# Performance work log

Hardware: AMD Instinct MI355X
Metric: run time of the kernel (lower is better)

The kernel has to match this reference:

```python
import jax, jax.numpy as jnp
import numpy as np


def _cdist(A, B):
    # Euclidean distance matrix via the norm trick: ||a-b||^2 = |a|^2 + |b|^2 - 2 a.b
    # A: (M, D), B: (N, D) -> (M, N). Avoids materializing (M, N, D).
    a2 = jnp.sum(A * A, axis=-1)[:, None]
    b2 = jnp.sum(B * B, axis=-1)[None, :]
    d2 = a2 + b2 - 2.0 * (A @ B.T)
    return jnp.sqrt(jnp.maximum(d2, 0.0))


def _multiquadric(x):
    return jnp.sqrt(x * x + 1.0)


def setup_inputs() -> dict:
    key = jax.random.key(0)
    k1, k2, k3 = jax.random.split(key, 3)
    M, N, D, K = 16384, 8192, 3, 64
    Xp = jax.random.normal(k1, (M, D), dtype=jnp.float32)
    X = jax.random.normal(k2, (N, D), dtype=jnp.float32)
    W = jax.random.normal(k3, (K, N), dtype=jnp.float32)  # solved weights self.M: (K, N)
    eps = jnp.ones((), dtype=jnp.float32)
    return {"Xp": Xp, "X": X, "W": W, "eps": eps}


def reference(Xp, X, W, eps):
    # dist: (M, N) pairwise distances, phi = kernel(eps * dist)
    dist = _cdist(Xp, X)
    phi = _multiquadric(eps * dist)
    # Solve.forward: matmul(W, phi^T)^T == phi @ W^T -> (M, K)
    return phi @ W.T
```

## Files before the change

kernel.cpp:

```cpp
#include <hip/hip_runtime.h>
#include <hip/hip_fp16.h>
#include <stdint.h>

#define M_ROWS 16384
#define N_PTS  8192
#define K_OUT  64

typedef _Float16       h2    __attribute__((ext_vector_type(2)));
typedef unsigned short u16x2 __attribute__((ext_vector_type(2)));
typedef _Float16       f16x8 __attribute__((ext_vector_type(8)));
typedef float          f32x4 __attribute__((ext_vector_type(4)));

union AF { f16x8 v; uint4 q; uint32_t u[4]; h2 h[4]; };

__device__ __forceinline__ h2 pkrtz2(float a, float b) {
    return __builtin_bit_cast(h2, __builtin_amdgcn_cvt_pkrtz(a, b));
}
__device__ __forceinline__ uint32_t pkrtz(float a, float b) {
    return __builtin_bit_cast(uint32_t, __builtin_amdgcn_cvt_pkrtz(a, b));
}

__device__ __forceinline__ h2 pk_sqrt_fast(h2 t, h2 mhf, h2 c15) {
    u16x2 u = __builtin_bit_cast(u16x2, t);
    u16x2 r0u = (u16x2){0x59BA, 0x59BA} - (u >> 1);
    h2 r0 = __builtin_bit_cast(h2, r0u);
    h2 y = t * r0;
    h2 p = y * r0;
    h2 k = __builtin_elementwise_fma(p, mhf, c15);
    return y * k;
}

__global__ __launch_bounds__(256) void rbf_prep(
    const float* __restrict__ Wf, const float* __restrict__ X,
    const float* __restrict__ epsp,
    uint4* __restrict__ Wt, uint32_t* __restrict__ Cx,
    uint32_t* __restrict__ Cy, uint32_t* __restrict__ Cz,
    uint32_t* __restrict__ Cc)
{
    const int bid = blockIdx.x, tid = threadIdx.x;
    if (bid < 256) {
        const int kt = tid >> 6, lane = tid & 63;
        const int l15 = lane & 15, g = lane >> 4;
        const int row = kt * 16 + l15;
        const int col = bid * 32 + g * 8;
        const float4* src = (const float4*)(Wf + row * N_PTS + col);
        const float4 w0 = src[0], w1 = src[1];
        uint4 p;
        p.x = pkrtz(w0.x, w0.y);
        p.y = pkrtz(w0.z, w0.w);
        p.z = pkrtz(w1.x, w1.y);
        p.w = pkrtz(w1.z, w1.w);
        Wt[(bid * 4 + kt) * 64 + lane] = p;
    } else {
        const int n = (bid - 256) * 256 + tid;
        const float e = *epsp;
        const float2 A = *(const float2*)(X + 6 * n);
        const float2 B = *(const float2*)(X + 6 * n + 2);
        const float2 C = *(const float2*)(X + 6 * n + 4);
        const float x0 = A.x * e, y0 = A.y * e, z0 = B.x * e;
        const float x1 = B.y * e, y1 = C.x * e, z1 = C.y * e;
        Cx[n] = pkrtz(-2.0f * x0, -2.0f * x1);
        Cy[n] = pkrtz(-2.0f * y0, -2.0f * y1);
        Cz[n] = pkrtz(-2.0f * z0, -2.0f * z1);
        Cc[n] = pkrtz(fmaf(x0, x0, fmaf(y0, y0, fmaf(z0, z0, 1.0f))),
                      fmaf(x1, x1, fmaf(y1, y1, fmaf(z1, z1, 1.0f))));
    }
}

__global__ __launch_bounds__(512, 4) void rbf_main(
    const float* __restrict__ Xp, const uint4* __restrict__ Wt,
    const uint32_t* __restrict__ Cx, const uint32_t* __restrict__ Cy,
    const uint32_t* __restrict__ Cz, const uint32_t* __restrict__ Cc,
    const float* __restrict__ epsp, float* __restrict__ out)
{
    __shared__ __align__(16) float sR[8 * 32 * 64];

    const int tid  = threadIdx.x;
    const int lane = tid & 63;
    const int wv   = tid >> 6;
    const int m    = lane & 15;
    const int g    = lane >> 4;

    const int rowbase = blockIdx.x * 32;

    const float e = *epsp;
    h2 pxk[2], pyk[2], pzk[2], aak[2];
    #pragma unroll
    for (int t = 0; t < 2; ++t) {
        const int r = rowbase + t * 16 + m;
        const float px = Xp[3 * r + 0] * e;
        const float py = Xp[3 * r + 1] * e;
        const float pz = Xp[3 * r + 2] * e;
        const float a  = fmaf(px, px, fmaf(py, py, pz * pz));
        pxk[t] = pkrtz2(px, px);
        pyk[t] = pkrtz2(py, py);
        pzk[t] = pkrtz2(pz, pz);
        aak[t] = pkrtz2(a, a);
    }
    const h2 mhf = {(_Float16)-0.5f, (_Float16)-0.5f};
    const h2 c15 = {(_Float16)1.5f, (_Float16)1.5f};

    f32x4 acc[2][4];
    #pragma unroll
    for (int t = 0; t < 2; ++t)
        #pragma unroll
        for (int kt = 0; kt < 4; ++kt)
            acc[t][kt] = (f32x4){0.f, 0.f, 0.f, 0.f};

    const uint32_t* cxp = Cx + wv * 512 + g * 4;
    const uint32_t* cyp = Cy + wv * 512 + g * 4;
    const uint32_t* czp = Cz + wv * 512 + g * 4;
    const uint32_t* ccp = Cc + wv * 512 + g * 4;
    const uint4*    wp  = Wt + wv * 8192 + lane;

    #pragma unroll 8
    for (int s = 0; s < 32; ++s) {
        const uint4 vx = *(const uint4*)(cxp + s * 16);
        const uint4 vy = *(const uint4*)(cyp + s * 16);
        const uint4 vz = *(const uint4*)(czp + s * 16);
        const uint4 vc = *(const uint4*)(ccp + s * 16);

        AF wf0, wf1, wf2, wf3;
        wf0.q = wp[s * 256];
        wf1.q = wp[s * 256 + 64];
        wf2.q = wp[s * 256 + 128];
        wf3.q = wp[s * 256 + 192];

        const h2 cx[4] = {__builtin_bit_cast(h2, vx.x), __builtin_bit_cast(h2, vx.y),
                          __builtin_bit_cast(h2, vx.z), __builtin_bit_cast(h2, vx.w)};
        const h2 cy[4] = {__builtin_bit_cast(h2, vy.x), __builtin_bit_cast(h2, vy.y),
                          __builtin_bit_cast(h2, vy.z), __builtin_bit_cast(h2, vy.w)};
        const h2 cz[4] = {__builtin_bit_cast(h2, vz.x), __builtin_bit_cast(h2, vz.y),
                          __builtin_bit_cast(h2, vz.z), __builtin_bit_cast(h2, vz.w)};
        const h2 cc[4] = {__builtin_bit_cast(h2, vc.x), __builtin_bit_cast(h2, vc.y),
                          __builtin_bit_cast(h2, vc.z), __builtin_bit_cast(h2, vc.w)};

        #pragma unroll
        for (int t = 0; t < 2; ++t) {
            AF af;
            #pragma unroll
            for (int j = 0; j < 4; ++j) {
                h2 d = cc[j] + aak[t];
                d = __builtin_elementwise_fma(pxk[t], cx[j], d);
                d = __builtin_elementwise_fma(pyk[t], cy[j], d);
                d = __builtin_elementwise_fma(pzk[t], cz[j], d);
                af.h[j] = pk_sqrt_fast(d, mhf, c15);
            }
            acc[t][0] = __builtin_amdgcn_mfma_f32_16x16x32_f16(af.v, wf0.v, acc[t][0], 0, 0, 0);
            acc[t][1] = __builtin_amdgcn_mfma_f32_16x16x32_f16(af.v, wf1.v, acc[t][1], 0, 0, 0);
            acc[t][2] = __builtin_amdgcn_mfma_f32_16x16x32_f16(af.v, wf2.v, acc[t][2], 0, 0, 0);
            acc[t][3] = __builtin_amdgcn_mfma_f32_16x16x32_f16(af.v, wf3.v, acc[t][3], 0, 0, 0);
        }
    }

    {
        float* base = sR + wv * 2048;
        #pragma unroll
        for (int t = 0; t < 2; ++t)
            #pragma unroll
            for (int kt = 0; kt < 4; ++kt)
                #pragma unroll
                for (int reg = 0; reg < 4; ++reg)
                    base[(t * 16 + g * 4 + reg) * 64 + kt * 16 + m] = acc[t][kt][reg];
    }
    __syncthreads();

    {
        const int row = tid >> 4;
        const int kq  = tid & 15;
        const float* p = sR + row * 64 + kq * 4;
        float4 s0 = *(const float4*)(p);
        #pragma unroll
        for (int w = 1; w < 8; ++w) {
            const float4 sw = *(const float4*)(p + w * 2048);
            s0.x += sw.x; s0.y += sw.y; s0.z += sw.z; s0.w += sw.w;
        }
        *(float4*)(out + (rowbase + row) * K_OUT + kq * 4) = s0;
    }
}

extern "C" void kernel_launch(void* const* d_in, const int* in_sizes, int n_in,
                              void* d_out, int out_size, void* d_ws, size_t ws_size,
                              hipStream_t stream) {
    (void)in_sizes; (void)n_in; (void)out_size; (void)ws_size;
    const float* Xp  = (const float*)d_in[0];
    const float* X   = (const float*)d_in[1];
    const float* Wf  = (const float*)d_in[2];
    const float* eps = (const float*)d_in[3];
    float* out = (float*)d_out;

    uint4*    Wt = (uint4*)d_ws;
    uint32_t* Cx = (uint32_t*)((char*)d_ws + (1u << 20));
    uint32_t* Cy = Cx + 4096;
    uint32_t* Cz = Cy + 4096;
    uint32_t* Cc = Cz + 4096;

    rbf_prep<<<dim3(272), dim3(256), 0, stream>>>(Wf, X, eps, Wt, Cx, Cy, Cz, Cc);
    rbf_main<<<dim3(M_ROWS / 32), dim3(512), 0, stream>>>(
        Xp, Wt, Cx, Cy, Cz, Cc, eps, out);
}
```

Baseline: 96.72 us.

## Split row tiles across waves using 1024-thread blocks

Each block now runs 16 waves, and each wave computes one 16-row tile over its N chunk instead of two tiles. The aim is to cut per-wave register pressure and raise the number of active waves for latency hiding. In exchange, W-fragment and coefficient loads are no longer reused across two row tiles, so per-MFMA memory traffic doubles. The final reduction uses only half the threads.

```diff
diff --git a/kernel.cpp b/kernel.cpp
--- a/kernel.cpp
+++ b/kernel.cpp
@@ -67,7 +67,7 @@
     }
 }
 
-__global__ __launch_bounds__(512, 4) void rbf_main(
+__global__ __launch_bounds__(1024, 8) void rbf_main(
     const float* __restrict__ Xp, const uint4* __restrict__ Wt,
     const uint32_t* __restrict__ Cx, const uint32_t* __restrict__ Cy,
     const uint32_t* __restrict__ Cz, const uint32_t* __restrict__ Cc,
@@ -78,42 +78,39 @@
     const int tid  = threadIdx.x;
     const int lane = tid & 63;
     const int wv   = tid >> 6;
+    const int rt   = wv & 1;
+    const int nc   = wv >> 1;
     const int m    = lane & 15;
     const int g    = lane >> 4;
 
-    const int rowbase = blockIdx.x * 32;
+    const int rowbase = blockIdx.x * 32 + rt * 16;
 
     const float e = *epsp;
-    h2 pxk[2], pyk[2], pzk[2], aak[2];
-    #pragma unroll
-    for (int t = 0; t < 2; ++t) {
-        const int r = rowbase + t * 16 + m;
+    h2 pxk, pyk, pzk, aak;
+    {
+        const int r = rowbase + m;
         const float px = Xp[3 * r + 0] * e;
         const float py = Xp[3 * r + 1] * e;
         const float pz = Xp[3 * r + 2] * e;
         const float a  = fmaf(px, px, fmaf(py, py, pz * pz));
-        pxk[t] = pkrtz2(px, px);
-        pyk[t] = pkrtz2(py, py);
-        pzk[t] = pkrtz2(pz, pz);
-        aak[t] = pkrtz2(a, a);
+        pxk = pkrtz2(px, px);
+        pyk = pkrtz2(py, py);
+        pzk = pkrtz2(pz, pz);
+        aak = pkrtz2(a, a);
     }
     const h2 mhf = {(_Float16)-0.5f, (_Float16)-0.5f};
     const h2 c15 = {(_Float16)1.5f, (_Float16)1.5f};
 
-    f32x4 acc[2][4];
-    #pragma unroll
-    for (int t = 0; t < 2; ++t)
-        #pragma unroll
-        for (int kt = 0; kt < 4; ++kt)
-            acc[t][kt] = (f32x4){0.f, 0.f, 0.f, 0.f};
+    f32x4 acc0 = {0.f, 0.f, 0.f, 0.f};
+    f32x4 acc1 = acc0, acc2 = acc0, acc3 = acc0;
 
-    const uint32_t* cxp = Cx + wv * 512 + g * 4;
-    const uint32_t* cyp = Cy + wv * 512 + g * 4;
-    const uint32_t* czp = Cz + wv * 512 + g * 4;
-    const uint32_t* ccp = Cc + wv * 512 + g * 4;
-    const uint4*    wp  = Wt + wv * 8192 + lane;
+    const uint32_t* cxp = Cx + nc * 512 + g * 4;
+    const uint32_t* cyp = Cy + nc * 512 + g * 4;
+    const uint32_t* czp = Cz + nc * 512 + g * 4;
+    const uint32_t* ccp = Cc + nc * 512 + g * 4;
+    const uint4*    wp  = Wt + nc * 8192 + lane;
 
-    #pragma unroll 8
+    #pragma unroll 4
     for (int s = 0; s < 32; ++s) {
         const uint4 vx = *(const uint4*)(cxp + s * 16);
         const uint4 vy = *(const uint4*)(cyp + s * 16);
@@ -135,37 +132,34 @@
         const h2 cc[4] = {__builtin_bit_cast(h2, vc.x), __builtin_bit_cast(h2, vc.y),
                           __builtin_bit_cast(h2, vc.z), __builtin_bit_cast(h2, vc.w)};
 
+        AF af;
         #pragma unroll
-        for (int t = 0; t < 2; ++t) {
-            AF af;
-            #pragma unroll
-            for (int j = 0; j < 4; ++j) {
-                h2 d = cc[j] + aak[t];
-                d = __builtin_elementwise_fma(pxk[t], cx[j], d);
-                d = __builtin_elementwise_fma(pyk[t], cy[j], d);
-                d = __builtin_elementwise_fma(pzk[t], cz[j], d);
-                af.h[j] = pk_sqrt_fast(d, mhf, c15);
-            }
-            acc[t][0] = __builtin_amdgcn_mfma_f32_16x16x32_f16(af.v, wf0.v, acc[t][0], 0, 0, 0);
-            acc[t][1] = __builtin_amdgcn_mfma_f32_16x16x32_f16(af.v, wf1.v, acc[t][1], 0, 0, 0);
-            acc[t][2] = __builtin_amdgcn_mfma_f32_16x16x32_f16(af.v, wf2.v, acc[t][2], 0, 0, 0);
-            acc[t][3] = __builtin_amdgcn_mfma_f32_16x16x32_f16(af.v, wf3.v, acc[t][3], 0, 0, 0);
+        for (int j = 0; j < 4; ++j) {
+            h2 d = cc[j] + aak;
+            d = __builtin_elementwise_fma(pxk, cx[j], d);
+            d = __builtin_elementwise_fma(pyk, cy[j], d);
+            d = __builtin_elementwise_fma(pzk, cz[j], d);
+            af.h[j] = pk_sqrt_fast(d, mhf, c15);
         }
+        acc0 = __builtin_amdgcn_mfma_f32_16x16x32_f16(af.v, wf0.v, acc0, 0, 0, 0);
+        acc1 = __builtin_amdgcn_mfma_f32_16x16x32_f16(af.v, wf1.v, acc1, 0, 0, 0);
+        acc2 = __builtin_amdgcn_mfma_f32_16x16x32_f16(af.v, wf2.v, acc2, 0, 0, 0);
+        acc3 = __builtin_amdgcn_mfma_f32_16x16x32_f16(af.v, wf3.v, acc3, 0, 0, 0);
     }
 
     {
-        float* base = sR + wv * 2048;
+        float* base = sR + nc * 2048 + (rt * 16 + g * 4) * 64 + m;
         #pragma unroll
-        for (int t = 0; t < 2; ++t)
-            #pragma unroll
-            for (int kt = 0; kt < 4; ++kt)
-                #pragma unroll
-                for (int reg = 0; reg < 4; ++reg)
-                    base[(t * 16 + g * 4 + reg) * 64 + kt * 16 + m] = acc[t][kt][reg];
+        for (int reg = 0; reg < 4; ++reg) {
+            base[reg * 64 +  0] = acc0[reg];
+            base[reg * 64 + 16] = acc1[reg];
+            base[reg * 64 + 32] = acc2[reg];
+            base[reg * 64 + 48] = acc3[reg];
+        }
     }
     __syncthreads();
 
-    {
+    if (tid < 512) {
         const int row = tid >> 4;
         const int kq  = tid & 15;
         const float* p = sR + row * 64 + kq * 4;
@@ -175,7 +169,7 @@
             const float4 sw = *(const float4*)(p + w * 2048);
             s0.x += sw.x; s0.y += sw.y; s0.z += sw.z; s0.w += sw.w;
         }
-        *(float4*)(out + (rowbase + row) * K_OUT + kq * 4) = s0;
+        *(float4*)(out + (blockIdx.x * 32 + row) * K_OUT + kq * 4) = s0;
     }
 }
 
@@ -196,6 +190,6 @@
     uint32_t* Cc = Cz + 4096;
 
     rbf_prep<<<dim3(272), dim3(256), 0, stream>>>(Wf, X, eps, Wt, Cx, Cy, Cz, Cc);
-    rbf_main<<<dim3(M_ROWS / 32), dim3(512), 0, stream>>>(
+    rbf_main<<<dim3(M_ROWS / 32), dim3(1024), 0, stream>>>(
         Xp, Wt, Cx, Cy, Cz, Cc, eps, out);
 }
```

Measured after the change: 128.4 us. +32.8%, slower.
